# Kernel optimization log

Measured on AMD Instinct MI355X. Metric: run time of the kernel, lower is better.

## Reference

```python
import jax, jax.numpy as jnp
import numpy as np

N = 100000      # points
M = 12500       # cluster centers
E0 = 1600000    # point-level edges
E1 = 400000     # cluster-level edges
F_IN = 4        # raw point feature dim (e.g. intensity + extras)
D = 64          # hidden feature width
N_CLASSES = 8


def setup_inputs() -> dict:
    key = jax.random.key(0)
    ks = jax.random.split(key, 20)
    s = 0.05
    d = {}
    d["features"] = jax.random.normal(ks[0], (N, F_IN), jnp.float32)
    d["points"] = jax.random.normal(ks[1], (N, 3), jnp.float32)
    d["cluster_centers"] = jax.random.normal(ks[2], (M, 3), jnp.float32)
    d["l0_edges"] = jax.random.randint(ks[3], (E0, 2), 0, N)
    d["l1_edges"] = jax.random.randint(ks[4], (E1, 2), 0, M)
    d["labels"] = jax.random.randint(ks[5], (N,), 0, M)
    # Feature_extract MLP
    d["W_fe"] = s * jax.random.normal(ks[6], (F_IN + 3, D), jnp.float32)
    d["b_fe"] = jnp.zeros((D,), jnp.float32)
    # 4 Mini_GNN layers (layer2, layer2_1, layer6, layer6_1), stacked
    d["mini_We"] = s * jax.random.normal(ks[7], (4, D + 3, D), jnp.float32)
    d["mini_be"] = jnp.zeros((4, D), jnp.float32)
    d["mini_Wu"] = s * jax.random.normal(ks[8], (4, D, D), jnp.float32)
    d["mini_bu"] = jnp.zeros((4, D), jnp.float32)
    # Mini_to_Large
    d["W_m1"] = s * jax.random.normal(ks[9], (D + 3, D), jnp.float32)
    d["b_m1"] = jnp.zeros((D,), jnp.float32)
    d["W_m2"] = s * jax.random.normal(ks[10], (D, D), jnp.float32)
    d["b_m2"] = jnp.zeros((D,), jnp.float32)
    # 2 GNN layers on cluster graph (layer4, layer4_1), stacked
    d["gnn_We"] = s * jax.random.normal(ks[11], (2, D + 3, D), jnp.float32)
    d["gnn_be"] = jnp.zeros((2, D), jnp.float32)
    d["gnn_Wu"] = s * jax.random.normal(ks[12], (2, D, D), jnp.float32)
    d["gnn_bu"] = jnp.zeros((2, D), jnp.float32)
    # Large_to_Mini
    d["W_l"] = s * jax.random.normal(ks[13], (D + 3, D), jnp.float32)
    d["b_l"] = jnp.zeros((D,), jnp.float32)
    # Classifier
    d["W_c"] = s * jax.random.normal(ks[14], (D, N_CLASSES), jnp.float32)
    d["b_c"] = jnp.zeros((N_CLASSES,), jnp.float32)
    return d


def _gnn_layer(feat, pos, edges, We, be, Wu, bu, n_nodes):
    """PointGNN-style layer: gather -> edge MLP -> scatter max -> update MLP -> residual."""
    src, dst = edges[:, 0], edges[:, 1]
    e_in = jnp.concatenate([pos[src] - pos[dst], feat[src]], axis=-1)  # [E, 3+D]
    h = jax.nn.relu(e_in @ We + be)                                     # [E, D]
    agg = jax.ops.segment_max(h, dst, num_segments=n_nodes)            # [n, D]
    agg = jnp.where(jnp.isneginf(agg), 0.0, agg)  # nodes with no in-edges -> 0
    return jax.nn.relu(agg @ Wu + bu) + feat


def reference(features, points, cluster_centers, l0_edges, l1_edges, labels,
              W_fe, b_fe, mini_We, mini_be, mini_Wu, mini_bu,
              W_m1, b_m1, W_m2, b_m2, gnn_We, gnn_be, gnn_Wu, gnn_bu,
              W_l, b_l, W_c, b_c):
    rel = points - cluster_centers[labels]  # [N, 3] point pos relative to its cluster
    # layer1: Feature_extract
    f1 = jax.nn.relu(jnp.concatenate([features, rel], -1) @ W_fe + b_fe)
    # layer2 / layer2_1: Mini_GNN (scatter max) on point graph
    f2 = _gnn_layer(f1, points, l0_edges, mini_We[0], mini_be[0], mini_Wu[0], mini_bu[0], N)
    f2_1 = _gnn_layer(f2, points, l0_edges, mini_We[1], mini_be[1], mini_Wu[1], mini_bu[1], N)
    # layer3: Mini_to_Large (scatter sum by labels)
    h = jax.nn.relu(jnp.concatenate([f2_1, rel], -1) @ W_m1 + b_m1)
    c = jax.ops.segment_sum(h, labels, num_segments=M)  # [M, D]
    f3 = jax.nn.relu(c @ W_m2 + b_m2)
    # layer4 / layer4_1: GNN (scatter max) on cluster graph
    f4 = _gnn_layer(f3, cluster_centers, l1_edges, gnn_We[0], gnn_be[0], gnn_Wu[0], gnn_bu[0], M)
    f4_1 = _gnn_layer(f4, cluster_centers, l1_edges, gnn_We[1], gnn_be[1], gnn_Wu[1], gnn_bu[1], M)
    # layer5: Large_to_Mini (gather by labels)
    f5 = jax.nn.relu(jnp.concatenate([f4_1[labels], rel], -1) @ W_l + b_l)
    # layer6 / layer6_1 with residual skips per call()
    f6 = _gnn_layer(f5, points, l0_edges, mini_We[2], mini_be[2], mini_Wu[2], mini_bu[2], N)
    f6 = f6 + f2_1
    f6_1 = _gnn_layer(f6, points, l0_edges, mini_We[3], mini_be[3], mini_Wu[3], mini_bu[3], N)
    final = f6_1 + f2
    return final @ W_c + b_c  # [N, N_CLASSES] per-point logits
```

## Files before the change

### kernel.cpp

```cpp
#include <hip/hip_runtime.h>

#define N_PTS   100000
#define M_CL    12500
#define E0_N    1600000
#define E1_N    400000

#define NB      256
#define BIN_CAP 32
#define RANGE0  391
#define RANGE1  49
#define BCAP0   8192
#define BCAP1   2048
#define BCAPL   1024

#define LSTR    72

typedef unsigned short ushortT;
typedef short  short8 __attribute__((ext_vector_type(8)));
typedef float  v4f    __attribute__((ext_vector_type(4)));
typedef _Float16 h2   __attribute__((ext_vector_type(2)));
typedef unsigned u4v  __attribute__((ext_vector_type(4)));

__device__ inline ushortT f2bf(float x){
  union{float f; unsigned u;} v; v.f = x;
  unsigned r = v.u + 0x7fffu + ((v.u >> 16) & 1u);
  return (ushortT)(r >> 16);
}
__device__ inline float bf2f(ushortT h){
  union{unsigned u; float f;} v; v.u = ((unsigned)h) << 16;
  return v.f;
}
__device__ inline ushortT f2h(float x){
  union{_Float16 h; ushortT u;} v; v.h = (_Float16)x;
  return v.u;
}
__device__ inline float h2f(ushortT u){
  union{ushortT u; _Float16 h;} v; v.u = u;
  return (float)v.h;
}
__device__ inline h2 pkmax(h2 a, h2 b){ return __builtin_elementwise_max(a, b); }
__device__ inline h2 u2h(unsigned u){ union{unsigned u; h2 h;} v{u}; return v.h; }


struct WSrc { const float* p[16]; };

__global__ __launch_bounds__(256) void k_init_wprep(WSrc s, ushortT* __restrict__ wt, ushortT* __restrict__ wtc,
                                                    int* c0, int* c1, int* cL){
  int blk = blockIdx.x;
  if (blk == 0){
    int t = threadIdx.x;
    c0[t] = t*BCAP0; c1[t] = t*BCAP1; cL[t] = t*BCAPL;
    return;
  }
  int slot = blk - 1;
  if (slot < 15){
    const float* src = s.p[slot];
    ushortT* dst = wt + slot*4096;
    for (int e=threadIdx.x; e<4096; e+=256){
      int nn = e>>6, kk = e&63;
      dst[e] = f2bf(src[kk*64+nn]);
    }
  } else {
    const float* src = s.p[15];
    for (int e=threadIdx.x; e<1024; e+=256){
      int nn = e>>6, kk = e&63;
      wtc[e] = (nn<8) ? f2bf(src[kk*8+nn]) : (ushortT)0;
    }
  }
}


template<int RANGE, bool LAB>
__device__ void bin_seg(const int* __restrict__ edges, int E,
                        int* __restrict__ bcur, unsigned* __restrict__ tmp,
                        int bid, int nblk,
                        unsigned* stage, int* scnt, int* sbase){
  int tid = threadIdx.x;
  int nchunks = (E + 2047) / 2048;
  for (int c = bid; c < nchunks; c += nblk){
    int base = c*2048;
    scnt[tid] = 0;
    __syncthreads();
    #pragma unroll
    for (int r=0;r<8;++r){
      int e = base + r*256 + tid;
      if (e < E){
        int s, d;
        if (LAB){ s = e; d = edges[e]; }
        else    { s = edges[2*e]; d = edges[2*e+1]; }
        int bk = d / RANGE;
        unsigned packed = ((unsigned)s << 11) | (unsigned)(d - bk*RANGE);
        int pos = atomicAdd(&scnt[bk], 1);
        if (pos < BIN_CAP) stage[bk*BIN_CAP+pos] = packed;
        else tmp[atomicAdd(&bcur[bk],1)] = packed;
      }
    }
    __syncthreads();
    {
      int nfl = scnt[tid]; if (nfl > BIN_CAP) nfl = BIN_CAP;
      sbase[tid] = atomicAdd(&bcur[tid], nfl);
    }
    __syncthreads();
    int wv = tid >> 6, ln = tid & 63;
    for (int bb=0; bb<32; ++bb){
      int bk = wv*64 + bb*2 + (ln>>5);
      int ent = ln & 31;
      int nf = scnt[bk]; if (nf > BIN_CAP) nf = BIN_CAP;
      if (ent < nf) tmp[sbase[bk]+ent] = stage[bk*BIN_CAP+ent];
    }
    __syncthreads();
  }
}

__global__ __launch_bounds__(256) void k_bin_all(const int* __restrict__ l0e, const int* __restrict__ l1e,
                                                 const int* __restrict__ labels,
                                                 int* bc0, int* bc1, int* bcL,
                                                 unsigned* t0, unsigned* t1, unsigned* tL){
  __shared__ unsigned stage[NB*BIN_CAP];
  __shared__ int scnt[NB];
  __shared__ int sbase[NB];
  int b = blockIdx.x;
  if (b < 256)      bin_seg<RANGE0,false>(l0e, E0_N, bc0, t0, b, 256, stage, scnt, sbase);
  else if (b < 452) bin_seg<RANGE1,false>(l1e, E1_N, bc1, t1, b-256, 196, stage, scnt, sbase);
  else              bin_seg<RANGE1,true >(labels, N_PTS, bcL, tL, b-452, 49, stage, scnt, sbase);
}

__global__ void k_scan_all(const int* c0, int* bb0, int* e0,
                           const int* c1, int* bb1, int* e1,
                           const int* cL, int* bbL, int* eL){
  const int* cur; int* bb; int* offe; int BC;
  if (blockIdx.x == 0){ cur=c0; bb=bb0; offe=e0; BC=BCAP0; }
  else if (blockIdx.x == 1){ cur=c1; bb=bb1; offe=e1; BC=BCAP1; }
  else { cur=cL; bb=bbL; offe=eL; BC=BCAPL; }
  int lane = threadIdx.x & 63;
  int base = lane*4;
  int v0 = cur[base+0] - (base+0)*BC;
  int v1 = cur[base+1] - (base+1)*BC;
  int v2 = cur[base+2] - (base+2)*BC;
  int v3 = cur[base+3] - (base+3)*BC;
  int psum = v0+v1+v2+v3, sc = psum;
  #pragma unroll
  for (int st=1; st<64; st<<=1){
    int x = __shfl_up(sc, st, 64);
    if (lane >= st) sc += x;
  }
  int ex = sc - psum;
  bb[base+0] = ex;
  bb[base+1] = ex + v0;
  bb[base+2] = ex + v0 + v1;
  bb[base+3] = ex + v0 + v1 + v2;
  if (lane == 63) *offe = sc;
}

template<int RANGE, int BCAP, int K>
__device__ void csr_build_seg(const unsigned* __restrict__ tmp, const int* __restrict__ bcur,
                              const int* __restrict__ bb, int n,
                              int* __restrict__ offs, int* __restrict__ csr,
                              int b, int* hist, int* part){
  int tid = threadIdx.x;
  int dlo = b*RANGE;
  int range = n - dlo; if (range > RANGE) range = RANGE; if (range < 0) range = 0;
  int cnt = bcur[b] - b*BCAP;
  for (int t=tid; t<RANGE; t+=256) hist[t] = 0;
  __syncthreads();
  const unsigned* sl = tmp + (size_t)b*BCAP;
  for (int j=tid; j<cnt; j+=256) atomicAdd(&hist[sl[j] & 2047u], 1);
  __syncthreads();
  int s = 0; int loc[K];
  #pragma unroll
  for (int kk=0; kk<K; ++kk){
    int idx = tid*K + kk;
    int v = (idx < RANGE) ? hist[idx] : 0;
    loc[kk] = s; s += v;
  }
  part[tid] = s; __syncthreads();
  int own = s;
  for (int st=1; st<256; st<<=1){
    int x = (tid >= st) ? part[tid-st] : 0;
    __syncthreads();
    part[tid] += x;
    __syncthreads();
  }
  int ebase = part[tid] - own;
  int gb = bb[b];
  __syncthreads();
  #pragma unroll
  for (int kk=0; kk<K; ++kk){
    int idx = tid*K + kk;
    if (idx < RANGE){
      int ex = ebase + loc[kk];
      if (idx < range) offs[dlo+idx] = gb + ex;
      hist[idx] = ex;
    }
  }
  __syncthreads();
  for (int j=tid; j<cnt; j+=256){
    unsigned p = sl[j];
    int pos = atomicAdd(&hist[p & 2047u], 1);
    csr[gb + pos] = (int)(p >> 11);
  }
}

__global__ __launch_bounds__(256) void k_build_all(
    const unsigned* t0, const int* bc0, const int* bb0, int* offs0, int* csr0,
    const unsigned* t1, const int* bc1, const int* bb1, int* offs1, int* csr1,
    const unsigned* tL, const int* bcL, const int* bbL, int* offsL, int* csrL){
  __shared__ int hist[RANGE0];
  __shared__ int part[256];
  int b = blockIdx.x;
  if (b < 256)      csr_build_seg<RANGE0,BCAP0,2>(t0, bc0, bb0, N_PTS, offs0, csr0, b, hist, part);
  else if (b < 512) csr_build_seg<RANGE1,BCAP1,1>(t1, bc1, bb1, M_CL, offs1, csr1, b-256, hist, part);
  else              csr_build_seg<RANGE1,BCAPL,1>(tL, bcL, bbL, M_CL, offsL, csrL, b-512, hist, part);
}


__global__ __launch_bounds__(256) void k_f1g(const float* __restrict__ features, const float* __restrict__ points,
                                             const float* __restrict__ centers, const int* __restrict__ labels,
                                             const float* __restrict__ W, const float* __restrict__ b,
                                             const ushortT* __restrict__ Wt2, const float* __restrict__ bias2,
                                             const float* __restrict__ Wr2,
                                             float* __restrict__ rel, ushortT* __restrict__ f1b,
                                             ushortT* __restrict__ gout, int n, int ntiles){
  __shared__ ushortT lds[4*16*LSTR];
  int tid = threadIdx.x;
  int lane = tid & 63, wslot = tid >> 6;
  int quad = lane >> 4, l15 = lane & 15;
  int gw = (blockIdx.x*256 + tid) >> 6;
  int nw = (gridDim.x*256) >> 6;
  float Wf0=W[0*64+lane], Wf1=W[1*64+lane], Wf2=W[2*64+lane], Wf3=W[3*64+lane];
  float wr0=W[4*64+lane], wr1=W[5*64+lane], wr2=W[6*64+lane];
  float bias=b[lane];
  short8 s0_0 = *(const short8*)(Wt2 + ( 0 + l15)*64 +  0 + quad*8);
  short8 s0_1 = *(const short8*)(Wt2 + ( 0 + l15)*64 + 32 + quad*8);
  short8 s1_0 = *(const short8*)(Wt2 + (16 + l15)*64 +  0 + quad*8);
  short8 s1_1 = *(const short8*)(Wt2 + (16 + l15)*64 + 32 + quad*8);
  short8 s2_0 = *(const short8*)(Wt2 + (32 + l15)*64 +  0 + quad*8);
  short8 s2_1 = *(const short8*)(Wt2 + (32 + l15)*64 + 32 + quad*8);
  short8 s3_0 = *(const short8*)(Wt2 + (48 + l15)*64 +  0 + quad*8);
  short8 s3_1 = *(const short8*)(Wt2 + (48 + l15)*64 + 32 + quad*8);
  float eb0 = bias2[l15], eb1 = bias2[16+l15], eb2 = bias2[32+l15], eb3 = bias2[48+l15];
  float e0c0=Wr2[0*64+l15], e0c1=Wr2[0*64+16+l15], e0c2=Wr2[0*64+32+l15], e0c3=Wr2[0*64+48+l15];
  float e1c0=Wr2[1*64+l15], e1c1=Wr2[1*64+16+l15], e1c2=Wr2[1*64+32+l15], e1c3=Wr2[1*64+48+l15];
  float e2c0=Wr2[2*64+l15], e2c1=Wr2[2*64+16+l15], e2c2=Wr2[2*64+32+l15], e2c3=Wr2[2*64+48+l15];

  for (int t=gw; t<ntiles; t+=nw){
    int i0 = t*16;
    for (int r=0;r<16;++r){
      int row = i0 + r;
      bool ok = row < n;
      int rr = ok ? row : n-1;
      int lb = labels[rr];
      float rx = points[rr*3+0]-centers[lb*3+0];
      float ry = points[rr*3+1]-centers[lb*3+1];
      float rz = points[rr*3+2]-centers[lb*3+2];
      float acc = bias + wr0*rx + wr1*ry + wr2*rz;
      acc += features[rr*4+0]*Wf0 + features[rr*4+1]*Wf1;
      acc += features[rr*4+2]*Wf2 + features[rr*4+3]*Wf3;
      acc = fmaxf(acc, 0.f);
      ushortT ab = f2bf(acc);
      if (ok){
        f1b[(size_t)row*64+lane] = ab;
        if (lane==0){ rel[row*3+0]=rx; rel[row*3+1]=ry; rel[row*3+2]=rz; }
      }
      lds[wslot*(16*LSTR) + r*LSTR + lane] = ab;
    }
    __builtin_amdgcn_wave_barrier();
    const ushortT* lp = lds + wslot*(16*LSTR) + l15*LSTR + quad*8;
    short8 sa0 = *(const short8*)(lp);
    short8 sa1 = *(const short8*)(lp + 32);
    __builtin_amdgcn_wave_barrier();
    v4f ec0 = {0.f,0.f,0.f,0.f}, ec1 = ec0, ec2 = ec0, ec3 = ec0;
    ec0 = __builtin_amdgcn_mfma_f32_16x16x32_bf16(sa0, s0_0, ec0, 0,0,0);
    ec1 = __builtin_amdgcn_mfma_f32_16x16x32_bf16(sa0, s1_0, ec1, 0,0,0);
    ec2 = __builtin_amdgcn_mfma_f32_16x16x32_bf16(sa0, s2_0, ec2, 0,0,0);
    ec3 = __builtin_amdgcn_mfma_f32_16x16x32_bf16(sa0, s3_0, ec3, 0,0,0);
    ec0 = __builtin_amdgcn_mfma_f32_16x16x32_bf16(sa1, s0_1, ec0, 0,0,0);
    ec1 = __builtin_amdgcn_mfma_f32_16x16x32_bf16(sa1, s1_1, ec1, 0,0,0);
    ec2 = __builtin_amdgcn_mfma_f32_16x16x32_bf16(sa1, s2_1, ec2, 0,0,0);
    ec3 = __builtin_amdgcn_mfma_f32_16x16x32_bf16(sa1, s3_1, ec3, 0,0,0);
    #pragma unroll
    for (int r=0;r<4;++r){
      int row = i0 + quad*4 + r;
      if (row < n){
        float vx=points[row*3+0], vy=points[row*3+1], vz=points[row*3+2];
        float g0 = ec0[r] + eb0 + vx*e0c0 + vy*e1c0 + vz*e2c0;
        float g1 = ec1[r] + eb1 + vx*e0c1 + vy*e1c1 + vz*e2c1;
        float g2 = ec2[r] + eb2 + vx*e0c2 + vy*e1c2 + vz*e2c2;
        float g3 = ec3[r] + eb3 + vx*e0c3 + vy*e1c3 + vz*e2c3;
        size_t base = (size_t)row*64 + l15;
        gout[base] = f2h(g0); gout[base+16] = f2h(g1); gout[base+32] = f2h(g2); gout[base+48] = f2h(g3);
      }
    }
  }
}


template<bool RELU, int NRES, bool USEREL, bool GATHER, bool OUT16, bool F16O, int EMODE, bool ERELU>
__global__ __launch_bounds__(256) void k_gemm(
    const ushortT* __restrict__ A, const ushortT* __restrict__ Wt,
    const float* __restrict__ bias, const float* __restrict__ Wr,
    const float* __restrict__ rel, const int* __restrict__ gidx,
    const ushortT* __restrict__ r1, const ushortT* __restrict__ r2,
    ushortT* __restrict__ out16,
    const ushortT* __restrict__ Wt2, const float* __restrict__ bias2,
    const float* __restrict__ Wr2, const float* __restrict__ vec2,
    void* __restrict__ eout,
    int n, int ntiles)
{
  constexpr int LDSZ = (EMODE>0) ? 4*16*LSTR : 4;
  __shared__ ushortT lds[LDSZ];
  int tid = threadIdx.x;
  int lane = tid & 63, wslot = tid >> 6;
  int quad = lane >> 4, l15 = lane & 15;
  int gw = (blockIdx.x*256 + tid) >> 6;
  int nw = (gridDim.x*256) >> 6;

  short8 bfr0_0 = *(const short8*)(Wt + ( 0 + l15)*64 +  0 + quad*8);
  short8 bfr0_1 = *(const short8*)(Wt + ( 0 + l15)*64 + 32 + quad*8);
  short8 bfr1_0 = *(const short8*)(Wt + (16 + l15)*64 +  0 + quad*8);
  short8 bfr1_1 = *(const short8*)(Wt + (16 + l15)*64 + 32 + quad*8);
  short8 bfr2_0 = *(const short8*)(Wt + (32 + l15)*64 +  0 + quad*8);
  short8 bfr2_1 = *(const short8*)(Wt + (32 + l15)*64 + 32 + quad*8);
  short8 bfr3_0 = *(const short8*)(Wt + (48 + l15)*64 +  0 + quad*8);
  short8 bfr3_1 = *(const short8*)(Wt + (48 + l15)*64 + 32 + quad*8);
  float bs0 = bias[ 0 + l15], bs1 = bias[16 + l15];
  float bs2 = bias[32 + l15], bs3 = bias[48 + l15];
  float w0c0=0,w0c1=0,w0c2=0,w0c3=0, w1c0=0,w1c1=0,w1c2=0,w1c3=0, w2c0=0,w2c1=0,w2c2=0,w2c3=0;
  if (USEREL){
    w0c0=Wr[0*64+l15]; w0c1=Wr[0*64+16+l15]; w0c2=Wr[0*64+32+l15]; w0c3=Wr[0*64+48+l15];
    w1c0=Wr[1*64+l15]; w1c1=Wr[1*64+16+l15]; w1c2=Wr[1*64+32+l15]; w1c3=Wr[1*64+48+l15];
    w2c0=Wr[2*64+l15]; w2c1=Wr[2*64+16+l15]; w2c2=Wr[2*64+32+l15]; w2c3=Wr[2*64+48+l15];
  }

  short8 s0_0{}, s0_1{}, s1_0{}, s1_1{}, s2_0{}, s2_1{}, s3_0{}, s3_1{};
  float eb0=0, eb1=0, eb2=0, eb3=0;
  float e0c0=0,e0c1=0,e0c2=0,e0c3=0, e1c0=0,e1c1=0,e1c2=0,e1c3=0, e2c0=0,e2c1=0,e2c2=0,e2c3=0;
  float ebias_c = 0.f;
  if (EMODE == 1){
    s0_0 = *(const short8*)(Wt2 + ( 0 + l15)*64 +  0 + quad*8);
    s0_1 = *(const short8*)(Wt2 + ( 0 + l15)*64 + 32 + quad*8);
    s1_0 = *(const short8*)(Wt2 + (16 + l15)*64 +  0 + quad*8);
    s1_1 = *(const short8*)(Wt2 + (16 + l15)*64 + 32 + quad*8);
    s2_0 = *(const short8*)(Wt2 + (32 + l15)*64 +  0 + quad*8);
    s2_1 = *(const short8*)(Wt2 + (32 + l15)*64 + 32 + quad*8);
    s3_0 = *(const short8*)(Wt2 + (48 + l15)*64 +  0 + quad*8);
    s3_1 = *(const short8*)(Wt2 + (48 + l15)*64 + 32 + quad*8);
    eb0 = bias2[l15]; eb1 = bias2[16+l15]; eb2 = bias2[32+l15]; eb3 = bias2[48+l15];
    e0c0=Wr2[0*64+l15]; e0c1=Wr2[0*64+16+l15]; e0c2=Wr2[0*64+32+l15]; e0c3=Wr2[0*64+48+l15];
    e1c0=Wr2[1*64+l15]; e1c1=Wr2[1*64+16+l15]; e1c2=Wr2[1*64+32+l15]; e1c3=Wr2[1*64+48+l15];
    e2c0=Wr2[2*64+l15]; e2c1=Wr2[2*64+16+l15]; e2c2=Wr2[2*64+32+l15]; e2c3=Wr2[2*64+48+l15];
  } else if (EMODE == 2){
    s0_0 = *(const short8*)(Wt2 + l15*64 +  0 + quad*8);
    s0_1 = *(const short8*)(Wt2 + l15*64 + 32 + quad*8);
    ebias_c = (l15 < 8) ? bias2[l15] : 0.f;
  }

  for (int t=gw; t<ntiles; t+=nw){
    int i0 = t*16;
    int rowA = i0 + l15; if (rowA >= n) rowA = n-1;
    if (GATHER) rowA = gidx[rowA];
    const ushortT* ap = A + (size_t)rowA*64 + quad*8;
    short8 a0 = *(const short8*)(ap);
    short8 a1 = *(const short8*)(ap + 32);
    v4f ac0 = {0.f,0.f,0.f,0.f}, ac1 = ac0, ac2 = ac0, ac3 = ac0;
    ac0 = __builtin_amdgcn_mfma_f32_16x16x32_bf16(a0, bfr0_0, ac0, 0,0,0);
    ac1 = __builtin_amdgcn_mfma_f32_16x16x32_bf16(a0, bfr1_0, ac1, 0,0,0);
    ac2 = __builtin_amdgcn_mfma_f32_16x16x32_bf16(a0, bfr2_0, ac2, 0,0,0);
    ac3 = __builtin_amdgcn_mfma_f32_16x16x32_bf16(a0, bfr3_0, ac3, 0,0,0);
    ac0 = __builtin_amdgcn_mfma_f32_16x16x32_bf16(a1, bfr0_1, ac0, 0,0,0);
    ac1 = __builtin_amdgcn_mfma_f32_16x16x32_bf16(a1, bfr1_1, ac1, 0,0,0);
    ac2 = __builtin_amdgcn_mfma_f32_16x16x32_bf16(a1, bfr2_1, ac2, 0,0,0);
    ac3 = __builtin_amdgcn_mfma_f32_16x16x32_bf16(a1, bfr3_1, ac3, 0,0,0);

    #pragma unroll
    for (int r=0;r<4;++r){
      int row = i0 + quad*4 + r;
      bool rowok = (row < n);
      float rx=0.f, ry=0.f, rz=0.f;
      if (USEREL && rowok){ rx=rel[row*3+0]; ry=rel[row*3+1]; rz=rel[row*3+2]; }
      float v0 = ac0[r] + bs0, v1 = ac1[r] + bs1, v2 = ac2[r] + bs2, v3 = ac3[r] + bs3;
      if (USEREL){
        v0 += rx*w0c0 + ry*w1c0 + rz*w2c0;
        v1 += rx*w0c1 + ry*w1c1 + rz*w2c1;
        v2 += rx*w0c2 + ry*w1c2 + rz*w2c2;
        v3 += rx*w0c3 + ry*w1c3 + rz*w2c3;
      }
      if (RELU){ v0=fmaxf(v0,0.f); v1=fmaxf(v1,0.f); v2=fmaxf(v2,0.f); v3=fmaxf(v3,0.f); }
      size_t base = (size_t)row*64 + l15;
      if (rowok){
        if (NRES>=1){
          v0 += bf2f(r1[base]); v1 += bf2f(r1[base+16]); v2 += bf2f(r1[base+32]); v3 += bf2f(r1[base+48]);
        }
        if (NRES>=2){
          v0 += bf2f(r2[base]); v1 += bf2f(r2[base+16]); v2 += bf2f(r2[base+32]); v3 += bf2f(r2[base+48]);
        }
        if (OUT16){
          if (F16O){
            out16[base] = f2h(v0); out16[base+16] = f2h(v1); out16[base+32] = f2h(v2); out16[base+48] = f2h(v3);
          } else {
            out16[base] = f2bf(v0); out16[base+16] = f2bf(v1); out16[base+32] = f2bf(v2); out16[base+48] = f2bf(v3);
          }
        }
      }
      if (EMODE > 0){
        int lb = wslot*(16*LSTR) + (quad*4+r)*LSTR + l15;
        lds[lb]      = f2bf(v0);
        lds[lb + 16] = f2bf(v1);
        lds[lb + 32] = f2bf(v2);
        lds[lb + 48] = f2bf(v3);
      }
    }

    if (EMODE > 0){
      __builtin_amdgcn_wave_barrier();
      const ushortT* lp = lds + wslot*(16*LSTR) + l15*LSTR + quad*8;
      short8 sa0 = *(const short8*)(lp);
      short8 sa1 = *(const short8*)(lp + 32);
      __builtin_amdgcn_wave_barrier();
      if (EMODE == 1){
        v4f ec0 = {0.f,0.f,0.f,0.f}, ec1 = ec0, ec2 = ec0, ec3 = ec0;
        ec0 = __builtin_amdgcn_mfma_f32_16x16x32_bf16(sa0, s0_0, ec0, 0,0,0);
        ec1 = __builtin_amdgcn_mfma_f32_16x16x32_bf16(sa0, s1_0, ec1, 0,0,0);
        ec2 = __builtin_amdgcn_mfma_f32_16x16x32_bf16(sa0, s2_0, ec2, 0,0,0);
        ec3 = __builtin_amdgcn_mfma_f32_16x16x32_bf16(sa0, s3_0, ec3, 0,0,0);
        ec0 = __builtin_amdgcn_mfma_f32_16x16x32_bf16(sa1, s0_1, ec0, 0,0,0);
        ec1 = __builtin_amdgcn_mfma_f32_16x16x32_bf16(sa1, s1_1, ec1, 0,0,0);
        ec2 = __builtin_amdgcn_mfma_f32_16x16x32_bf16(sa1, s2_1, ec2, 0,0,0);
        ec3 = __builtin_amdgcn_mfma_f32_16x16x32_bf16(sa1, s3_1, ec3, 0,0,0);
        ushortT* eo = (ushortT*)eout;
        #pragma unroll
        for (int r=0;r<4;++r){
          int row = i0 + quad*4 + r;
          if (row < n){
            float vx=vec2[row*3+0], vy=vec2[row*3+1], vz=vec2[row*3+2];
            float g0 = ec0[r] + eb0 + vx*e0c0 + vy*e1c0 + vz*e2c0;
            float g1 = ec1[r] + eb1 + vx*e0c1 + vy*e1c1 + vz*e2c1;
            float g2 = ec2[r] + eb2 + vx*e0c2 + vy*e1c2 + vz*e2c2;
            float g3 = ec3[r] + eb3 + vx*e0c3 + vy*e1c3 + vz*e2c3;
            if (ERELU){ g0=fmaxf(g0,0.f); g1=fmaxf(g1,0.f); g2=fmaxf(g2,0.f); g3=fmaxf(g3,0.f); }
            size_t base = (size_t)row*64 + l15;
            eo[base] = f2h(g0); eo[base+16] = f2h(g1); eo[base+32] = f2h(g2); eo[base+48] = f2h(g3);
          }
        }
      } else {
        v4f ec = {0.f,0.f,0.f,0.f};
        ec = __builtin_amdgcn_mfma_f32_16x16x32_bf16(sa0, s0_0, ec, 0,0,0);
        ec = __builtin_amdgcn_mfma_f32_16x16x32_bf16(sa1, s0_1, ec, 0,0,0);
        if (l15 < 8){
          float* eo = (float*)eout;
          #pragma unroll
          for (int r=0;r<4;++r){
            int row = i0 + quad*4 + r;
            if (row < n) eo[(size_t)row*8 + l15] = ec[r] + ebias_c;
          }
        }
      }
    }
  }
}


__global__ __launch_bounds__(256) void k_edge_agg(const int* __restrict__ offs, const int* __restrict__ csr,
                                                  const float* __restrict__ pos, const ushortT* __restrict__ g,
                                                  const float* __restrict__ Wp, ushortT* __restrict__ agg, int n){
  int lane = threadIdx.x & 63;
  int grp = lane >> 3, d8 = lane & 7;
  int gbase = lane & 56;
  int gw = (blockIdx.x*256 + threadIdx.x) >> 6;
  int nw = (gridDim.x*256) >> 6;
  const u4v* g4 = (const u4v*)g;
  float2 w0[4], w1[4], w2[4];
  #pragma unroll
  for (int q=0;q<4;++q){
    w0[q] = *(const float2*)(Wp + 0*64 + d8*8 + 2*q);
    w1[q] = *(const float2*)(Wp + 1*64 + d8*8 + 2*q);
    w2[q] = *(const float2*)(Wp + 2*64 + d8*8 + 2*q);
  }
  const h2 NEGBIG = {(_Float16)-60000.f, (_Float16)-60000.f};
  int n8 = (n+7) >> 3;
  for (int ii=gw; ii<n8; ii+=nw){
    int i0 = ii*8;
    int ig = i0 + grp; bool ok = ig < n; if (!ok) ig = n-1;
    int b = offs[ig], e = offs[ig+1];
    int cnt = e - b, c1 = cnt - 1;
    int mx = cnt;
    mx = max(mx, __shfl_xor(mx, 8, 64));
    mx = max(mx, __shfl_xor(mx, 16, 64));
    mx = max(mx, __shfl_xor(mx, 32, 64));
    h2 m0=NEGBIG, m1=NEGBIG, m2=NEGBIG, m3=NEGBIG;
    for (int J=0; J<mx; J+=8){
      if (J < cnt){
        int sv = csr[b + min(J + d8, c1)];
        #pragma unroll
        for (int jj=0; jj<8; ++jj){
          int s = __shfl(sv, gbase + jj, 64);
          u4v u = g4[(size_t)s*8 + d8];
          m0 = pkmax(m0, u2h(u.x));
          m1 = pkmax(m1, u2h(u.y));
          m2 = pkmax(m2, u2h(u.z));
          m3 = pkmax(m3, u2h(u.w));
        }
      }
    }
    float px = pos[ig*3+0], py = pos[ig*3+1], pz = pos[ig*3+2];
    u4v outv;
    {
      float sA = w0[0].x*px + w1[0].x*py + w2[0].x*pz;
      float sB = w0[0].y*px + w1[0].y*py + w2[0].y*pz;
      outv.x = (unsigned)f2bf(fmaxf((float)m0.x - sA, 0.f)) |
               ((unsigned)f2bf(fmaxf((float)m0.y - sB, 0.f)) << 16);
    }
    {
      float sA = w0[1].x*px + w1[1].x*py + w2[1].x*pz;
      float sB = w0[1].y*px + w1[1].y*py + w2[1].y*pz;
      outv.y = (unsigned)f2bf(fmaxf((float)m1.x - sA, 0.f)) |
               ((unsigned)f2bf(fmaxf((float)m1.y - sB, 0.f)) << 16);
    }
    {
      float sA = w0[2].x*px + w1[2].x*py + w2[2].x*pz;
      float sB = w0[2].y*px + w1[2].y*py + w2[2].y*pz;
      outv.z = (unsigned)f2bf(fmaxf((float)m2.x - sA, 0.f)) |
               ((unsigned)f2bf(fmaxf((float)m2.y - sB, 0.f)) << 16);
    }
    {
      float sA = w0[3].x*px + w1[3].x*py + w2[3].x*pz;
      float sB = w0[3].y*px + w1[3].y*py + w2[3].y*pz;
      outv.w = (unsigned)f2bf(fmaxf((float)m3.x - sA, 0.f)) |
               ((unsigned)f2bf(fmaxf((float)m3.y - sB, 0.f)) << 16);
    }
    if (ok) ((u4v*)agg)[(size_t)ig*8 + d8] = outv;
  }
}


__global__ __launch_bounds__(256) void k_seg_gather(const int* __restrict__ offs, const int* __restrict__ csr,
                                                    const ushortT* __restrict__ h, ushortT* __restrict__ c, int m){
  int lane = threadIdx.x & 63;
  int wv = (blockIdx.x*256 + threadIdx.x) >> 6;
  if (wv >= m) return;
  int b = offs[wv], e = offs[wv+1];
  float acc = 0.f;
  for (int k=b; k<e; ++k){
    int i = csr[k];
    acc += h2f(h[(size_t)i*64+lane]);
  }
  c[(size_t)wv*64+lane] = f2bf(acc);
}


extern "C" void kernel_launch(void* const* d_in, const int* in_sizes, int n_in,
                              void* d_out, int out_size, void* d_ws, size_t ws_size,
                              hipStream_t stream){
  const float* features = (const float*)d_in[0];
  const float* points   = (const float*)d_in[1];
  const float* centers  = (const float*)d_in[2];
  const int*   l0e      = (const int*)d_in[3];
  const int*   l1e      = (const int*)d_in[4];
  const int*   labels   = (const int*)d_in[5];
  const float* W_fe = (const float*)d_in[6];
  const float* b_fe = (const float*)d_in[7];
  const float* mWe  = (const float*)d_in[8];
  const float* mbe  = (const float*)d_in[9];
  const float* mWu  = (const float*)d_in[10];
  const float* mbu  = (const float*)d_in[11];
  const float* W_m1 = (const float*)d_in[12];
  const float* b_m1 = (const float*)d_in[13];
  const float* W_m2 = (const float*)d_in[14];
  const float* b_m2 = (const float*)d_in[15];
  const float* gWe  = (const float*)d_in[16];
  const float* gbe  = (const float*)d_in[17];
  const float* gWu  = (const float*)d_in[18];
  const float* gbu  = (const float*)d_in[19];
  const float* W_l  = (const float*)d_in[20];
  const float* b_l  = (const float*)d_in[21];
  const float* W_c  = (const float*)d_in[22];
  const float* b_c  = (const float*)d_in[23];
  float* out = (float*)d_out;

  char* w = (char*)d_ws;
  size_t off = 0;
  auto alloc = [&](size_t bytes)->void*{
    void* p = (void*)(w + off);
    off = (off + bytes + 255) & ~(size_t)255;
    return p;
  };
  float* rel  = (float*)alloc((size_t)N_PTS*3*4);
  ushortT* UF1 = (ushortT*)alloc((size_t)N_PTS*64*2);
  ushortT* UF2 = (ushortT*)alloc((size_t)N_PTS*64*2);
  ushortT* UF21= (ushortT*)alloc((size_t)N_PTS*64*2);
  ushortT* UF5 = (ushortT*)alloc((size_t)N_PTS*64*2);
  ushortT* UF6 = (ushortT*)alloc((size_t)N_PTS*64*2);
  ushortT* gbuf= (ushortT*)alloc((size_t)N_PTS*64*2);
  ushortT* abuf= (ushortT*)alloc((size_t)N_PTS*64*2);
  ushortT* cb_b= (ushortT*)alloc((size_t)M_CL*64*2);
  ushortT* UF3 = (ushortT*)alloc((size_t)M_CL*64*2);
  ushortT* UF4 = (ushortT*)alloc((size_t)M_CL*64*2);
  ushortT* cg_b= (ushortT*)alloc((size_t)M_CL*64*2);
  ushortT* cagg_b = (ushortT*)alloc((size_t)M_CL*64*2);
  ushortT* f41_b  = (ushortT*)alloc((size_t)M_CL*64*2);
  ushortT* wt  = (ushortT*)alloc((size_t)15*4096*2);
  ushortT* wtc = (ushortT*)alloc((size_t)1024*2);
  int* offs0 = (int*)alloc((size_t)(N_PTS+1)*4);
  int* csr0  = (int*)alloc((size_t)E0_N*4);
  int* offs1 = (int*)alloc((size_t)(M_CL+1)*4);
  int* csr1  = (int*)alloc((size_t)E1_N*4);
  int* offsL = (int*)alloc((size_t)(M_CL+1)*4);
  int* csrL  = (int*)alloc((size_t)N_PTS*4);
  unsigned* tmp0 = (unsigned*)alloc((size_t)NB*BCAP0*4);
  unsigned* tmp1 = (unsigned*)alloc((size_t)NB*BCAP1*4);
  unsigned* tmpL = (unsigned*)alloc((size_t)NB*BCAPL*4);
  int* bcur0 = (int*)alloc(NB*4);
  int* bcur1 = (int*)alloc(NB*4);
  int* bcurL = (int*)alloc(NB*4);
  int* bb0   = (int*)alloc(NB*4);
  int* bb1   = (int*)alloc(NB*4);
  int* bbL   = (int*)alloc(NB*4);
  (void)ws_size; (void)in_sizes; (void)n_in; (void)out_size;

  const int NT_N = (N_PTS+15)/16;
  const int NT_M = (M_CL +15)/16;
  const int GBG_N = 1563;
  const int GBG_M = 196;
  const int GB_N  = 3125;

  WSrc ws{};
  ws.p[0]=mWu+0*4096; ws.p[1]=mWu+1*4096; ws.p[2]=mWu+2*4096; ws.p[3]=mWu+3*4096;
  ws.p[4]=W_m2; ws.p[5]=gWu+0*4096; ws.p[6]=gWu+1*4096;
  ws.p[7]=mWe+0*4288+192; ws.p[8]=mWe+1*4288+192; ws.p[9]=mWe+2*4288+192; ws.p[10]=mWe+3*4288+192;
  ws.p[11]=W_m1; ws.p[12]=W_l; ws.p[13]=gWe+0*4288+192; ws.p[14]=gWe+1*4288+192;
  ws.p[15]=W_c;
  k_init_wprep<<<17, 256, 0, stream>>>(ws, wt, wtc, bcur0, bcur1, bcurL);
  k_bin_all<<<501, 256, 0, stream>>>(l0e, l1e, labels, bcur0, bcur1, bcurL, tmp0, tmp1, tmpL);
  k_scan_all<<<3, 64, 0, stream>>>(bcur0, bb0, offs0+N_PTS, bcur1, bb1, offs1+M_CL, bcurL, bbL, offsL+M_CL);
  k_build_all<<<768, 256, 0, stream>>>(tmp0, bcur0, bb0, offs0, csr0,
                                       tmp1, bcur1, bb1, offs1, csr1,
                                       tmpL, bcurL, bbL, offsL, csrL);

  k_f1g<<<GBG_N, 256, 0, stream>>>(features, points, centers, labels, W_fe, b_fe,
      wt+7*4096, mbe+0, mWe+0*4288, rel, UF1, gbuf, N_PTS, NT_N);

  k_edge_agg<<<GB_N,256,0,stream>>>(offs0, csr0, points, gbuf, mWe+0*4288, abuf, N_PTS);
  k_gemm<true,1,false,false,true,false,1,false><<<GBG_N,256,0,stream>>>(abuf, wt+0*4096, mbu+0,
      nullptr, nullptr, nullptr, UF1, nullptr, UF2,
      wt+8*4096, mbe+64, mWe+1*4288, points, gbuf, N_PTS, NT_N);
  k_edge_agg<<<GB_N,256,0,stream>>>(offs0, csr0, points, gbuf, mWe+1*4288, abuf, N_PTS);
  k_gemm<true,1,false,false,true,false,1,true><<<GBG_N,256,0,stream>>>(abuf, wt+1*4096, mbu+64,
      nullptr, nullptr, nullptr, UF2, nullptr, UF21,
      wt+11*4096, b_m1, W_m1+4096, rel, gbuf, N_PTS, NT_N);
  k_seg_gather<<<(M_CL*64+255)/256, 256, 0, stream>>>(offsL, csrL, gbuf, cb_b, M_CL);
  k_gemm<true,0,false,false,true,false,1,false><<<GBG_M,256,0,stream>>>(cb_b, wt+4*4096, b_m2,
      nullptr, nullptr, nullptr, nullptr, nullptr, UF3,
      wt+13*4096, gbe+0, gWe+0*4288, centers, cg_b, M_CL, NT_M);
  k_edge_agg<<<GBG_M,256,0,stream>>>(offs1, csr1, centers, cg_b, gWe+0*4288, cagg_b, M_CL);
  k_gemm<true,1,false,false,true,false,1,false><<<GBG_M,256,0,stream>>>(cagg_b, wt+5*4096, gbu+0,
      nullptr, nullptr, nullptr, UF3, nullptr, UF4,
      wt+14*4096, gbe+64, gWe+1*4288, centers, cg_b, M_CL, NT_M);
  k_edge_agg<<<GBG_M,256,0,stream>>>(offs1, csr1, centers, cg_b, gWe+1*4288, cagg_b, M_CL);
  k_gemm<true,1,false,false,true,false,0,false><<<GBG_M,256,0,stream>>>(cagg_b, wt+6*4096, gbu+64,
      nullptr, nullptr, nullptr, UF4, nullptr, f41_b,
      nullptr, nullptr, nullptr, nullptr, nullptr, M_CL, NT_M);
  k_gemm<true,0,true,true,true,false,1,false><<<GBG_N,256,0,stream>>>(f41_b, wt+12*4096, b_l,
      W_l+4096, rel, labels, nullptr, nullptr, UF5,
      wt+9*4096, mbe+128, mWe+2*4288, points, gbuf, N_PTS, NT_N);
  k_edge_agg<<<GB_N,256,0,stream>>>(offs0, csr0, points, gbuf, mWe+2*4288, abuf, N_PTS);
  k_gemm<true,2,false,false,true,false,1,false><<<GBG_N,256,0,stream>>>(abuf, wt+2*4096, mbu+128,
      nullptr, nullptr, nullptr, UF5, UF21, UF6,
      wt+10*4096, mbe+192, mWe+3*4288, points, gbuf, N_PTS, NT_N);
  k_edge_agg<<<GB_N,256,0,stream>>>(offs0, csr0, points, gbuf, mWe+3*4288, abuf, N_PTS);
  k_gemm<true,2,false,false,false,false,2,false><<<GBG_N,256,0,stream>>>(abuf, wt+3*4096, mbu+192,
      nullptr, nullptr, nullptr, UF6, UF2, nullptr,
      wtc, b_c, nullptr, nullptr, out, N_PTS, NT_N);
}
```

Before: 479.6 us.

## Store features in four 16-column planes for cache-local edge gathers

Every 64-wide feature buffer moves from row-major [N,64] to four planes of [N,16], and all producers and consumers are rewritten to index the planes. The edge aggregation kernel now gives each block one plane, with two lanes per node and 32 nodes per wave, so the random source gathers touch a quarter of the bytes per pass and each plane has a better chance of staying in cache. It also switches the CSR, offset and position loads to nontemporal hints. In exchange, each gather row is only 32 bytes instead of a full 128-byte row, and the CSR indices are reread once per plane.

```diff
diff --git a/kernel.cpp b/kernel.cpp
--- a/kernel.cpp
+++ b/kernel.cpp
@@ -1,4 +1,5 @@
 #include <hip/hip_runtime.h>
+
 
 #define N_PTS   100000
 #define M_CL    12500
@@ -227,6 +228,7 @@
   int quad = lane >> 4, l15 = lane & 15;
   int gw = (blockIdx.x*256 + tid) >> 6;
   int nw = (gridDim.x*256) >> 6;
+  size_t n16 = (size_t)n*16;
   float Wf0=W[0*64+lane], Wf1=W[1*64+lane], Wf2=W[2*64+lane], Wf3=W[3*64+lane];
   float wr0=W[4*64+lane], wr1=W[5*64+lane], wr2=W[6*64+lane];
   float bias=b[lane];
@@ -259,7 +261,7 @@
       acc = fmaxf(acc, 0.f);
       ushortT ab = f2bf(acc);
       if (ok){
-        f1b[(size_t)row*64+lane] = ab;
+        f1b[(size_t)quad*n16 + (size_t)row*16 + l15] = ab;
         if (lane==0){ rel[row*3+0]=rx; rel[row*3+1]=ry; rel[row*3+2]=rz; }
       }
       lds[wslot*(16*LSTR) + r*LSTR + lane] = ab;
@@ -287,8 +289,8 @@
         float g1 = ec1[r] + eb1 + vx*e0c1 + vy*e1c1 + vz*e2c1;
         float g2 = ec2[r] + eb2 + vx*e0c2 + vy*e1c2 + vz*e2c2;
         float g3 = ec3[r] + eb3 + vx*e0c3 + vy*e1c3 + vz*e2c3;
-        size_t base = (size_t)row*64 + l15;
-        gout[base] = f2h(g0); gout[base+16] = f2h(g1); gout[base+32] = f2h(g2); gout[base+48] = f2h(g3);
+        size_t pb = (size_t)row*16 + l15;
+        gout[pb] = f2h(g0); gout[pb+n16] = f2h(g1); gout[pb+2*n16] = f2h(g2); gout[pb+3*n16] = f2h(g3);
       }
     }
   }
@@ -305,7 +307,7 @@
     const ushortT* __restrict__ Wt2, const float* __restrict__ bias2,
     const float* __restrict__ Wr2, const float* __restrict__ vec2,
     void* __restrict__ eout,
-    int n, int ntiles)
+    int n, int na, int ntiles)
 {
   constexpr int LDSZ = (EMODE>0) ? 4*16*LSTR : 4;
   __shared__ ushortT lds[LDSZ];
@@ -314,6 +316,8 @@
   int quad = lane >> 4, l15 = lane & 15;
   int gw = (blockIdx.x*256 + tid) >> 6;
   int nw = (gridDim.x*256) >> 6;
+  size_t n16  = (size_t)n*16;
+  size_t na16 = (size_t)na*16;
 
   short8 bfr0_0 = *(const short8*)(Wt + ( 0 + l15)*64 +  0 + quad*8);
   short8 bfr0_1 = *(const short8*)(Wt + ( 0 + l15)*64 + 32 + quad*8);
@@ -359,9 +363,9 @@
     int i0 = t*16;
     int rowA = i0 + l15; if (rowA >= n) rowA = n-1;
     if (GATHER) rowA = gidx[rowA];
-    const ushortT* ap = A + (size_t)rowA*64 + quad*8;
+    const ushortT* ap = A + (size_t)(quad>>1)*na16 + (size_t)rowA*16 + (quad&1)*8;
     short8 a0 = *(const short8*)(ap);
-    short8 a1 = *(const short8*)(ap + 32);
+    short8 a1 = *(const short8*)(ap + 2*na16);
     v4f ac0 = {0.f,0.f,0.f,0.f}, ac1 = ac0, ac2 = ac0, ac3 = ac0;
     ac0 = __builtin_amdgcn_mfma_f32_16x16x32_bf16(a0, bfr0_0, ac0, 0,0,0);
     ac1 = __builtin_amdgcn_mfma_f32_16x16x32_bf16(a0, bfr1_0, ac1, 0,0,0);
@@ -386,19 +390,19 @@
         v3 += rx*w0c3 + ry*w1c3 + rz*w2c3;
       }
       if (RELU){ v0=fmaxf(v0,0.f); v1=fmaxf(v1,0.f); v2=fmaxf(v2,0.f); v3=fmaxf(v3,0.f); }
-      size_t base = (size_t)row*64 + l15;
+      size_t pb = (size_t)row*16 + l15;
       if (rowok){
         if (NRES>=1){
-          v0 += bf2f(r1[base]); v1 += bf2f(r1[base+16]); v2 += bf2f(r1[base+32]); v3 += bf2f(r1[base+48]);
+          v0 += bf2f(r1[pb]); v1 += bf2f(r1[pb+n16]); v2 += bf2f(r1[pb+2*n16]); v3 += bf2f(r1[pb+3*n16]);
         }
         if (NRES>=2){
-          v0 += bf2f(r2[base]); v1 += bf2f(r2[base+16]); v2 += bf2f(r2[base+32]); v3 += bf2f(r2[base+48]);
+          v0 += bf2f(r2[pb]); v1 += bf2f(r2[pb+n16]); v2 += bf2f(r2[pb+2*n16]); v3 += bf2f(r2[pb+3*n16]);
         }
         if (OUT16){
           if (F16O){
-            out16[base] = f2h(v0); out16[base+16] = f2h(v1); out16[base+32] = f2h(v2); out16[base+48] = f2h(v3);
+            out16[pb] = f2h(v0); out16[pb+n16] = f2h(v1); out16[pb+2*n16] = f2h(v2); out16[pb+3*n16] = f2h(v3);
           } else {
-            out16[base] = f2bf(v0); out16[base+16] = f2bf(v1); out16[base+32] = f2bf(v2); out16[base+48] = f2bf(v3);
+            out16[pb] = f2bf(v0); out16[pb+n16] = f2bf(v1); out16[pb+2*n16] = f2bf(v2); out16[pb+3*n16] = f2bf(v3);
           }
         }
       }
@@ -438,8 +442,8 @@
             float g2 = ec2[r] + eb2 + vx*e0c2 + vy*e1c2 + vz*e2c2;
             float g3 = ec3[r] + eb3 + vx*e0c3 + vy*e1c3 + vz*e2c3;
             if (ERELU){ g0=fmaxf(g0,0.f); g1=fmaxf(g1,0.f); g2=fmaxf(g2,0.f); g3=fmaxf(g3,0.f); }
-            size_t base = (size_t)row*64 + l15;
-            eo[base] = f2h(g0); eo[base+16] = f2h(g1); eo[base+32] = f2h(g2); eo[base+48] = f2h(g3);
+            size_t pb = (size_t)row*16 + l15;
+            eo[pb] = f2h(g0); eo[pb+n16] = f2h(g1); eo[pb+2*n16] = f2h(g2); eo[pb+3*n16] = f2h(g3);
           }
         }
       } else {
@@ -462,89 +466,108 @@
 
 __global__ __launch_bounds__(256) void k_edge_agg(const int* __restrict__ offs, const int* __restrict__ csr,
                                                   const float* __restrict__ pos, const ushortT* __restrict__ g,
-                                                  const float* __restrict__ Wp, ushortT* __restrict__ agg, int n){
-  int lane = threadIdx.x & 63;
-  int grp = lane >> 3, d8 = lane & 7;
-  int gbase = lane & 56;
-  int gw = (blockIdx.x*256 + threadIdx.x) >> 6;
-  int nw = (gridDim.x*256) >> 6;
-  const u4v* g4 = (const u4v*)g;
+                                                  const float* __restrict__ Wp, ushortT* __restrict__ agg,
+                                                  int n, int n32){
+  int tid = threadIdx.x;
+  int lane = tid & 63, wslot = tid >> 6;
+  int grp = lane >> 1, h = lane & 1;
+  int gbase = lane & 62;
+  int b7 = blockIdx.x & 7;
+  int plane = b7 >> 1;
+  int bp = ((blockIdx.x >> 3) << 1) + (b7 & 1);
+  int ii = bp*4 + wslot;
+  if (ii >= n32) return;
+  const ushortT* gp = g + (size_t)plane*n*16;
+  int c0 = plane*16 + h*8;
   float2 w0[4], w1[4], w2[4];
   #pragma unroll
   for (int q=0;q<4;++q){
-    w0[q] = *(const float2*)(Wp + 0*64 + d8*8 + 2*q);
-    w1[q] = *(const float2*)(Wp + 1*64 + d8*8 + 2*q);
-    w2[q] = *(const float2*)(Wp + 2*64 + d8*8 + 2*q);
+    w0[q] = *(const float2*)(Wp + 0*64 + c0 + 2*q);
+    w1[q] = *(const float2*)(Wp + 1*64 + c0 + 2*q);
+    w2[q] = *(const float2*)(Wp + 2*64 + c0 + 2*q);
   }
   const h2 NEGBIG = {(_Float16)-60000.f, (_Float16)-60000.f};
-  int n8 = (n+7) >> 3;
-  for (int ii=gw; ii<n8; ii+=nw){
-    int i0 = ii*8;
-    int ig = i0 + grp; bool ok = ig < n; if (!ok) ig = n-1;
-    int b = offs[ig], e = offs[ig+1];
-    int cnt = e - b, c1 = cnt - 1;
-    int mx = cnt;
-    mx = max(mx, __shfl_xor(mx, 8, 64));
-    mx = max(mx, __shfl_xor(mx, 16, 64));
-    mx = max(mx, __shfl_xor(mx, 32, 64));
-    h2 m0=NEGBIG, m1=NEGBIG, m2=NEGBIG, m3=NEGBIG;
-    for (int J=0; J<mx; J+=8){
-      if (J < cnt){
-        int sv = csr[b + min(J + d8, c1)];
-        #pragma unroll
-        for (int jj=0; jj<8; ++jj){
-          int s = __shfl(sv, gbase + jj, 64);
-          u4v u = g4[(size_t)s*8 + d8];
-          m0 = pkmax(m0, u2h(u.x));
-          m1 = pkmax(m1, u2h(u.y));
-          m2 = pkmax(m2, u2h(u.z));
-          m3 = pkmax(m3, u2h(u.w));
-        }
-      }
-    }
-    float px = pos[ig*3+0], py = pos[ig*3+1], pz = pos[ig*3+2];
-    u4v outv;
-    {
-      float sA = w0[0].x*px + w1[0].x*py + w2[0].x*pz;
-      float sB = w0[0].y*px + w1[0].y*py + w2[0].y*pz;
-      outv.x = (unsigned)f2bf(fmaxf((float)m0.x - sA, 0.f)) |
-               ((unsigned)f2bf(fmaxf((float)m0.y - sB, 0.f)) << 16);
-    }
-    {
-      float sA = w0[1].x*px + w1[1].x*py + w2[1].x*pz;
-      float sB = w0[1].y*px + w1[1].y*py + w2[1].y*pz;
-      outv.y = (unsigned)f2bf(fmaxf((float)m1.x - sA, 0.f)) |
-               ((unsigned)f2bf(fmaxf((float)m1.y - sB, 0.f)) << 16);
-    }
-    {
-      float sA = w0[2].x*px + w1[2].x*py + w2[2].x*pz;
-      float sB = w0[2].y*px + w1[2].y*py + w2[2].y*pz;
-      outv.z = (unsigned)f2bf(fmaxf((float)m2.x - sA, 0.f)) |
-               ((unsigned)f2bf(fmaxf((float)m2.y - sB, 0.f)) << 16);
-    }
-    {
-      float sA = w0[3].x*px + w1[3].x*py + w2[3].x*pz;
-      float sB = w0[3].y*px + w1[3].y*py + w2[3].y*pz;
-      outv.w = (unsigned)f2bf(fmaxf((float)m3.x - sA, 0.f)) |
-               ((unsigned)f2bf(fmaxf((float)m3.y - sB, 0.f)) << 16);
-    }
-    if (ok) ((u4v*)agg)[(size_t)ig*8 + d8] = outv;
-  }
+  int ig = ii*32 + grp;
+  bool ok = ig < n;
+  int igc = ok ? ig : (n-1);
+  int bofs = 0, cnt = 0;
+  if (ok){
+    bofs = __builtin_nontemporal_load(offs + ig);
+    cnt  = __builtin_nontemporal_load(offs + ig + 1) - bofs;
+  }
+  int mx = cnt;
+  mx = max(mx, __shfl_xor(mx,  2, 64));
+  mx = max(mx, __shfl_xor(mx,  4, 64));
+  mx = max(mx, __shfl_xor(mx,  8, 64));
+  mx = max(mx, __shfl_xor(mx, 16, 64));
+  mx = max(mx, __shfl_xor(mx, 32, 64));
+  h2 m0=NEGBIG, m1=NEGBIG, m2=NEGBIG, m3=NEGBIG;
+  for (int J=0; J<mx; J+=8){
+    int sv0=0, sv1=0, sv2=0, sv3=0;
+    if (J+h   < cnt) sv0 = __builtin_nontemporal_load(csr + bofs + J + h);
+    if (J+h+2 < cnt) sv1 = __builtin_nontemporal_load(csr + bofs + J + h + 2);
+    if (J+h+4 < cnt) sv2 = __builtin_nontemporal_load(csr + bofs + J + h + 4);
+    if (J+h+6 < cnt) sv3 = __builtin_nontemporal_load(csr + bofs + J + h + 6);
+    #pragma unroll
+    for (int jj=0; jj<8; ++jj){
+      int sv = (jj<2) ? sv0 : (jj<4) ? sv1 : (jj<6) ? sv2 : sv3;
+      if (J + jj < cnt){
+        int s = __shfl(sv, gbase + (jj & 1), 64);
+        u4v u = *(const u4v*)(gp + (size_t)s*16 + h*8);
+        m0 = pkmax(m0, u2h(u.x));
+        m1 = pkmax(m1, u2h(u.y));
+        m2 = pkmax(m2, u2h(u.z));
+        m3 = pkmax(m3, u2h(u.w));
+      }
+    }
+  }
+  float px = __builtin_nontemporal_load(pos + igc*3 + 0);
+  float py = __builtin_nontemporal_load(pos + igc*3 + 1);
+  float pz = __builtin_nontemporal_load(pos + igc*3 + 2);
+  u4v outv;
+  {
+    float sA = w0[0].x*px + w1[0].x*py + w2[0].x*pz;
+    float sB = w0[0].y*px + w1[0].y*py + w2[0].y*pz;
+    outv.x = (unsigned)f2bf(fmaxf((float)m0.x - sA, 0.f)) |
+             ((unsigned)f2bf(fmaxf((float)m0.y - sB, 0.f)) << 16);
+  }
+  {
+    float sA = w0[1].x*px + w1[1].x*py + w2[1].x*pz;
+    float sB = w0[1].y*px + w1[1].y*py + w2[1].y*pz;
+    outv.y = (unsigned)f2bf(fmaxf((float)m1.x - sA, 0.f)) |
+             ((unsigned)f2bf(fmaxf((float)m1.y - sB, 0.f)) << 16);
+  }
+  {
+    float sA = w0[2].x*px + w1[2].x*py + w2[2].x*pz;
+    float sB = w0[2].y*px + w1[2].y*py + w2[2].y*pz;
+    outv.z = (unsigned)f2bf(fmaxf((float)m2.x - sA, 0.f)) |
+             ((unsigned)f2bf(fmaxf((float)m2.y - sB, 0.f)) << 16);
+  }
+  {
+    float sA = w0[3].x*px + w1[3].x*py + w2[3].x*pz;
+    float sB = w0[3].y*px + w1[3].y*py + w2[3].y*pz;
+    outv.w = (unsigned)f2bf(fmaxf((float)m3.x - sA, 0.f)) |
+             ((unsigned)f2bf(fmaxf((float)m3.y - sB, 0.f)) << 16);
+  }
+  if (ok) __builtin_nontemporal_store(outv, (u4v*)(agg + ((size_t)plane*n + ig)*16 + h*8));
 }
 
 
 __global__ __launch_bounds__(256) void k_seg_gather(const int* __restrict__ offs, const int* __restrict__ csr,
-                                                    const ushortT* __restrict__ h, ushortT* __restrict__ c, int m){
+                                                    const ushortT* __restrict__ h, ushortT* __restrict__ c,
+                                                    int m, int nh){
   int lane = threadIdx.x & 63;
+  int l15 = lane & 15, q = lane >> 4;
   int wv = (blockIdx.x*256 + threadIdx.x) >> 6;
   if (wv >= m) return;
   int b = offs[wv], e = offs[wv+1];
   float acc = 0.f;
+  const ushortT* hp = h + (size_t)q*nh*16 + l15;
   for (int k=b; k<e; ++k){
     int i = csr[k];
-    acc += h2f(h[(size_t)i*64+lane]);
-  }
-  c[(size_t)wv*64+lane] = f2bf(acc);
+    acc += h2f(hp[(size_t)i*16]);
+  }
+  c[((size_t)q*m + wv)*16 + l15] = f2bf(acc);
 }
 
 
@@ -621,7 +644,10 @@
   const int NT_M = (M_CL +15)/16;
   const int GBG_N = 1563;
   const int GBG_M = 196;
-  const int GB_N  = 3125;
+  const int GB_AGG_N = 3128;
+  const int N32_N    = 3125;
+  const int GB_AGG_M = 392;
+  const int N32_M    = 391;
 
   WSrc ws{};
   ws.p[0]=mWu+0*4096; ws.p[1]=mWu+1*4096; ws.p[2]=mWu+2*4096; ws.p[3]=mWu+3*4096;
@@ -639,35 +665,35 @@
   k_f1g<<<GBG_N, 256, 0, stream>>>(features, points, centers, labels, W_fe, b_fe,
       wt+7*4096, mbe+0, mWe+0*4288, rel, UF1, gbuf, N_PTS, NT_N);
 
-  k_edge_agg<<<GB_N,256,0,stream>>>(offs0, csr0, points, gbuf, mWe+0*4288, abuf, N_PTS);
+  k_edge_agg<<<GB_AGG_N,256,0,stream>>>(offs0, csr0, points, gbuf, mWe+0*4288, abuf, N_PTS, N32_N);
   k_gemm<true,1,false,false,true,false,1,false><<<GBG_N,256,0,stream>>>(abuf, wt+0*4096, mbu+0,
       nullptr, nullptr, nullptr, UF1, nullptr, UF2,
-      wt+8*4096, mbe+64, mWe+1*4288, points, gbuf, N_PTS, NT_N);
-  k_edge_agg<<<GB_N,256,0,stream>>>(offs0, csr0, points, gbuf, mWe+1*4288, abuf, N_PTS);
+      wt+8*4096, mbe+64, mWe+1*4288, points, gbuf, N_PTS, N_PTS, NT_N);
+  k_edge_agg<<<GB_AGG_N,256,0,stream>>>(offs0, csr0, points, gbuf, mWe+1*4288, abuf, N_PTS, N32_N);
   k_gemm<true,1,false,false,true,false,1,true><<<GBG_N,256,0,stream>>>(abuf, wt+1*4096, mbu+64,
       nullptr, nullptr, nullptr, UF2, nullptr, UF21,
-      wt+11*4096, b_m1, W_m1+4096, rel, gbuf, N_PTS, NT_N);
-  k_seg_gather<<<(M_CL*64+255)/256, 256, 0, stream>>>(offsL, csrL, gbuf, cb_b, M_CL);
+      wt+11*4096, b_m1, W_m1+4096, rel, gbuf, N_PTS, N_PTS, NT_N);
+  k_seg_gather<<<(M_CL*64+255)/256, 256, 0, stream>>>(offsL, csrL, gbuf, cb_b, M_CL, N_PTS);
   k_gemm<true,0,false,false,true,false,1,false><<<GBG_M,256,0,stream>>>(cb_b, wt+4*4096, b_m2,
       nullptr, nullptr, nullptr, nullptr, nullptr, UF3,
-      wt+13*4096, gbe+0, gWe+0*4288, centers, cg_b, M_CL, NT_M);
-  k_edge_agg<<<GBG_M,256,0,stream>>>(offs1, csr1, centers, cg_b, gWe+0*4288, cagg_b, M_CL);
+      wt+13*4096, gbe+0, gWe+0*4288, centers, cg_b, M_CL, M_CL, NT_M);
+  k_edge_agg<<<GB_AGG_M,256,0,stream>>>(offs1, csr1, centers, cg_b, gWe+0*4288, cagg_b, M_CL, N32_M);
   k_gemm<true,1,false,false,true,false,1,false><<<GBG_M,256,0,stream>>>(cagg_b, wt+5*4096, gbu+0,
       nullptr, nullptr, nullptr, UF3, nullptr, UF4,
-      wt+14*4096, gbe+64, gWe+1*4288, centers, cg_b, M_CL, NT_M);
-  k_edge_agg<<<GBG_M,256,0,stream>>>(offs1, csr1, centers, cg_b, gWe+1*4288, cagg_b, M_CL);
+      wt+14*4096, gbe+64, gWe+1*4288, centers, cg_b, M_CL, M_CL, NT_M);
+  k_edge_agg<<<GB_AGG_M,256,0,stream>>>(offs1, csr1, centers, cg_b, gWe+1*4288, cagg_b, M_CL, N32_M);
   k_gemm<true,1,false,false,true,false,0,false><<<GBG_M,256,0,stream>>>(cagg_b, wt+6*4096, gbu+64,
       nullptr, nullptr, nullptr, UF4, nullptr, f41_b,
-      nullptr, nullptr, nullptr, nullptr, nullptr, M_CL, NT_M);
+      nullptr, nullptr, nullptr, nullptr, nullptr, M_CL, M_CL, NT_M);
   k_gemm<true,0,true,true,true,false,1,false><<<GBG_N,256,0,stream>>>(f41_b, wt+12*4096, b_l,
       W_l+4096, rel, labels, nullptr, nullptr, UF5,
-      wt+9*4096, mbe+128, mWe+2*4288, points, gbuf, N_PTS, NT_N);
-  k_edge_agg<<<GB_N,256,0,stream>>>(offs0, csr0, points, gbuf, mWe+2*4288, abuf, N_PTS);
+      wt+9*4096, mbe+128, mWe+2*4288, points, gbuf, N_PTS, M_CL, NT_N);
+  k_edge_agg<<<GB_AGG_N,256,0,stream>>>(offs0, csr0, points, gbuf, mWe+2*4288, abuf, N_PTS, N32_N);
   k_gemm<true,2,false,false,true,false,1,false><<<GBG_N,256,0,stream>>>(abuf, wt+2*4096, mbu+128,
       nullptr, nullptr, nullptr, UF5, UF21, UF6,
-      wt+10*4096, mbe+192, mWe+3*4288, points, gbuf, N_PTS, NT_N);
-  k_edge_agg<<<GB_N,256,0,stream>>>(offs0, csr0, points, gbuf, mWe+3*4288, abuf, N_PTS);
+      wt+10*4096, mbe+192, mWe+3*4288, points, gbuf, N_PTS, N_PTS, NT_N);
+  k_edge_agg<<<GB_AGG_N,256,0,stream>>>(offs0, csr0, points, gbuf, mWe+3*4288, abuf, N_PTS, N32_N);
   k_gemm<true,2,false,false,false,false,2,false><<<GBG_N,256,0,stream>>>(abuf, wt+3*4096, mbu+192,
       nullptr, nullptr, nullptr, UF6, UF2, nullptr,
-      wtc, b_c, nullptr, nullptr, out, N_PTS, NT_N);
-}
+      wtc, b_c, nullptr, nullptr, out, N_PTS, N_PTS, NT_N);
+}
```

New measurement: 652.2 us. +36.0%, slower.
